# Performance work log

Hardware: AMD Instinct MI355X
Metric: run time of the kernel (lower is better)

Reference implementation:

```python
import jax, jax.numpy as jnp
import numpy as np

N_NODES = 50000
N_EDGES = 500000
D_MODEL = 128
D_INNER = 256
N_EXPERT = 64
TOP_K = 2
CAP_FACTOR = 2  # capacity factor for expert dispatch (fastmoe has no drop; factor 2 is ample for ~uniform gates)
BN_EPS = 1e-5


def setup_inputs() -> dict:
    key = jax.random.key(0)
    ks = jax.random.split(key, 12)
    d, h, E = D_MODEL, D_INNER, N_EXPERT
    return {
        "feats": jax.random.normal(ks[0], (N_NODES, d), jnp.float32),
        "edge_src": jax.random.randint(ks[1], (N_EDGES,), 0, N_NODES),
        "edge_dst": jax.random.randint(ks[2], (N_EDGES,), 0, N_NODES),
        "W_conv": jax.random.normal(ks[3], (d, d), jnp.float32) / np.sqrt(d),
        "b_conv": jnp.zeros((d,), jnp.float32),
        "gate_W": jax.random.normal(ks[4], (d, E), jnp.float32) / np.sqrt(d),
        "gate_b": jnp.zeros((E,), jnp.float32),
        "W1": jax.random.normal(ks[5], (E, d, h), jnp.float32) / np.sqrt(d),
        "b1": jnp.zeros((E, h), jnp.float32),
        "W2": jax.random.normal(ks[6], (E, h, d), jnp.float32) / np.sqrt(h),
        "b2": jnp.zeros((E, d), jnp.float32),
        "bn_gamma": jnp.ones((d,), jnp.float32),
        "bn_beta": jnp.zeros((d,), jnp.float32),
    }


def _gcn_conv(feats, edge_src, edge_dst, W_conv, b_conv):
    # symmetric-normalized sum aggregation over edge list
    n = feats.shape[0]
    ones = jnp.ones_like(edge_dst, dtype=feats.dtype)
    deg = jax.ops.segment_sum(ones, edge_dst, num_segments=n)
    deg = jnp.maximum(deg, 1.0)
    inv_sqrt = jax.lax.rsqrt(deg)
    norm = inv_sqrt[edge_src] * inv_sqrt[edge_dst]          # [Ed]
    msgs = feats[edge_src] * norm[:, None]                  # [Ed, d]
    agg = jax.ops.segment_sum(msgs, edge_dst, num_segments=n)
    return agg @ W_conv + b_conv


def _moe_ffn(x, gate_W, gate_b, W1, b1, W2, b2):
    # fastmoe NaiveGate: top-k of linear gate, softmax over the top-k scores
    T, d = x.shape
    E, h = W1.shape[0], W1.shape[2]
    scores = x @ gate_W + gate_b                            # [T, E]
    topv, topi = jax.lax.top_k(scores, TOP_K)               # [T, k]
    gw = jax.nn.softmax(topv, axis=-1)                      # [T, k]

    P = T * TOP_K
    eid = topi.reshape(P)                                   # expert id per (token, slot)
    x_rep = jnp.repeat(x, TOP_K, axis=0)                    # [P, d]

    onehot = jax.nn.one_hot(eid, E, dtype=jnp.int32)        # [P, E]
    pos = jnp.sum(jnp.cumsum(onehot, axis=0) * onehot, axis=-1) - 1  # rank within expert
    C = CAP_FACTOR * int(np.ceil(P / E))
    valid = pos < C
    slot = eid * C + jnp.where(valid, pos, 0)               # [P]

    buf = jnp.zeros((E * C, d), x.dtype).at[slot].add(
        jnp.where(valid[:, None], x_rep, 0.0))
    buf = buf.reshape(E, C, d)
    hact = jax.nn.gelu(jnp.einsum('ecd,edh->ech', buf, W1) + b1[:, None, :],
                       approximate=False)
    y = jnp.einsum('ech,ehd->ecd', hact, W2) + b2[:, None, :]
    y_pairs = y.reshape(E * C, d)[slot] * valid[:, None].astype(x.dtype)  # [P, d]
    y_pairs = y_pairs.reshape(T, TOP_K, d)
    return jnp.einsum('tk,tkd->td', gw, y_pairs)


def _batchnorm(x, gamma, beta):
    mean = jnp.mean(x, axis=0)
    var = jnp.mean(jnp.square(x - mean), axis=0)  # biased, as torch BN training
    return (x - mean) * jax.lax.rsqrt(var + BN_EPS) * gamma + beta


def reference(feats, edge_src, edge_dst, W_conv, b_conv, gate_W, gate_b,
              W1, b1, W2, b2, bn_gamma, bn_beta):
    new_feats = _gcn_conv(feats, edge_src, edge_dst, W_conv, b_conv)
    core = _moe_ffn(new_feats, gate_W, gate_b, W1, b1, W2, b2)
    # dropout p=0.0 -> identity; BN(inp + core_out)
    return _batchnorm(new_feats + core, bn_gamma, bn_beta)
```

## Files before the change

kernel.cpp:

```cpp
#include <hip/hip_runtime.h>
#include <math.h>

#define N_NODES 50000
#define N_EDGES 500000
#define D 128
#define H 256
#define NE 64
#define TOPK 2
#define NPAIR (N_NODES * TOPK)
#define CAP 3126
#define TILE_R 32
#define BQ 16
#define BN_NBLK 128
#define BN_ROWS ((N_NODES + BN_NBLK - 1) / BN_NBLK)

typedef __attribute__((ext_vector_type(8))) short s16x8;
typedef __attribute__((ext_vector_type(4))) float f32x4;

__device__ __forceinline__ unsigned short f2bf(float f) {
    unsigned u = __float_as_uint(f);
    unsigned r = (u + 0x7fffu + ((u >> 16) & 1u)) >> 16;
    return (unsigned short)r;
}
__device__ __forceinline__ float bf2f(unsigned short u) {
    return __uint_as_float(((unsigned)u) << 16);
}

__device__ __forceinline__ float gelu_f(float x) {
    float u = 0.70710678118654752f * x;
    float au = fabsf(u);
    float t = 1.0f / fmaf(0.3275911f, au, 1.0f);
    float poly = t * fmaf(t, fmaf(t, fmaf(t, fmaf(t, 1.061405429f, -1.453152027f),
                      1.421413741f), -0.284496736f), 0.254829592f);
    float e = __expf(-u * u);
    float erfa = 1.0f - poly * e;
    float erfu = copysignf(erfa, u);
    return 0.5f * x * (1.0f + erfu);
}

#define DOT2(s, c, xx, ww) {                      \
    float p_ = (xx) * (ww);                       \
    float e1_ = fmaf((xx), (ww), -p_);            \
    float t_ = (s) + p_;                          \
    float z_ = t_ - (s);                          \
    float e2_ = ((s) - (t_ - z_)) + (p_ - z_);    \
    (s) = t_;                                     \
    (c) += e1_ + e2_; }

#define TSUM(s, c, pp) {                          \
    float p_ = (pp);                              \
    float t_ = (s) + p_;                          \
    float z_ = t_ - (s);                          \
    float e2_ = ((s) - (t_ - z_)) + (p_ - z_);    \
    (s) = t_;                                     \
    (c) += e2_; }

#define KAH(s, c, pp) {                           \
    float y_ = (pp) - (c);                        \
    float t_ = (s) + y_;                          \
    (c) = (t_ - (s)) - y_;                        \
    (s) = t_; }

__global__ void k_deg(const int* __restrict__ dst, int* __restrict__ deg) {
    int i = blockIdx.x * blockDim.x + threadIdx.x;
    if (i < N_EDGES) atomicAdd(&deg[dst[i]], 1);
}

__global__ void k_invsqrt(const int* __restrict__ deg, float* __restrict__ invs) {
    int i = blockIdx.x * blockDim.x + threadIdx.x;
    if (i < N_NODES) {
        double d = (double)deg[i];
        if (d < 1.0) d = 1.0;
        invs[i] = (float)(1.0 / sqrt(d));
    }
}

__global__ __launch_bounds__(1024) void k_scan(const int* __restrict__ deg,
                                               int* __restrict__ rowptr) {
    __shared__ int sh[1024];
    int t = threadIdx.x;
    const int chunk = (N_NODES + 1023) / 1024;
    int lo = t * chunk;
    int hi = min(lo + chunk, N_NODES);
    int s = 0;
    for (int i = lo; i < hi; i++) s += deg[i];
    sh[t] = s;
    __syncthreads();
    for (int off = 1; off < 1024; off <<= 1) {
        int v = (t >= off) ? sh[t - off] : 0;
        __syncthreads();
        sh[t] += v;
        __syncthreads();
    }
    int run = (t == 0) ? 0 : sh[t - 1];
    for (int i = lo; i < hi; i++) { rowptr[i] = run; run += deg[i]; }
    if (t == 1023) rowptr[N_NODES] = run;
}

__global__ void k_scatter(const int* __restrict__ src, const int* __restrict__ dst,
                          const int* __restrict__ rowptr, int* __restrict__ cursor,
                          int* __restrict__ csr) {
    int e = blockIdx.x * blockDim.x + threadIdx.x;
    if (e >= N_EDGES) return;
    int d = dst[e];
    int pos = atomicAdd(&cursor[d], 1);
    csr[rowptr[d] + pos] = src[e];
}

__global__ __launch_bounds__(256) void k_gather(const float* __restrict__ feats,
                                                const int* __restrict__ rowptr,
                                                const int* __restrict__ csr,
                                                const float* __restrict__ invs,
                                                float* __restrict__ agg) {
    int node = blockIdx.x * 4 + (threadIdx.x >> 6);
    if (node >= N_NODES) return;
    int lane = threadIdx.x & 63;
    int beg = rowptr[node], end = rowptr[node + 1];
    float wd = invs[node];
    float sx = 0.f, cx = 0.f, sy = 0.f, cy = 0.f;
    int i = beg;
    for (; i + 4 <= end; i += 4) {
        int s0 = csr[i], s1 = csr[i + 1], s2 = csr[i + 2], s3 = csr[i + 3];
        float n0 = invs[s0] * wd, n1 = invs[s1] * wd;
        float n2 = invs[s2] * wd, n3 = invs[s3] * wd;
        float2 f0 = ((const float2*)(feats + (size_t)s0 * D))[lane];
        float2 f1 = ((const float2*)(feats + (size_t)s1 * D))[lane];
        float2 f2 = ((const float2*)(feats + (size_t)s2 * D))[lane];
        float2 f3 = ((const float2*)(feats + (size_t)s3 * D))[lane];
        KAH(sx, cx, n0 * f0.x); KAH(sy, cy, n0 * f0.y);
        KAH(sx, cx, n1 * f1.x); KAH(sy, cy, n1 * f1.y);
        KAH(sx, cx, n2 * f2.x); KAH(sy, cy, n2 * f2.y);
        KAH(sx, cx, n3 * f3.x); KAH(sy, cy, n3 * f3.y);
    }
    for (; i < end; i++) {
        int s = csr[i];
        float nrm = invs[s] * wd;
        float2 f = ((const float2*)(feats + (size_t)s * D))[lane];
        KAH(sx, cx, nrm * f.x);
        KAH(sy, cy, nrm * f.y);
    }
    ((float2*)(agg + (size_t)node * D))[lane] = make_float2(sx, sy);
}

__global__ __launch_bounds__(256) void k_conv(const float* __restrict__ agg,
                                              const float* __restrict__ W,
                                              const float* __restrict__ bias,
                                              float* __restrict__ out) {
    __shared__ float Wl[D * D];
    __shared__ float xl[TILE_R * D];
    int r0 = blockIdx.x * TILE_R;
    int rows = min(TILE_R, N_NODES - r0);
    for (int i = threadIdx.x; i < D * D / 4; i += 256)
        ((float4*)Wl)[i] = ((const float4*)W)[i];
    for (int i = threadIdx.x; i < rows * 32; i += 256) {
        int r = i >> 5, q = i & 31;
        ((float4*)(xl + r * D))[q] = ((const float4*)(agg + (size_t)(r0 + r) * D))[q];
    }
    __syncthreads();
    int c = threadIdx.x & 127;
    int half = threadIdx.x >> 7;
    float acc[16];
#pragma unroll
    for (int j = 0; j < 16; j++) acc[j] = 0.f;
    for (int k = 0; k < D; k++) {
        float w = Wl[k * D + c];
#pragma unroll
        for (int j = 0; j < 16; j++) acc[j] += xl[(half + j * 2) * D + k] * w;
    }
    float b = bias[c];
#pragma unroll
    for (int j = 0; j < 16; j++) {
        int r = half + j * 2;
        if (r < rows) out[(size_t)(r0 + r) * D + c] = acc[j] + b;
    }
}

__global__ __launch_bounds__(256, 4) void k_gate(const float* __restrict__ nf,
                                                 const float* __restrict__ gW,
                                                 const float* __restrict__ gb,
                                                 float* __restrict__ gwout,
                                                 int* __restrict__ topi,
                                                 int* __restrict__ rcnt,
                                                 int* __restrict__ redo) {
    __shared__ float Wl[D * NE];
    __shared__ float xsh[16 * D];
    for (int i = threadIdx.x; i < D * NE / 4; i += 256)
        ((float4*)Wl)[i] = ((const float4*)gW)[i];
    int t_base = blockIdx.x * 16;
    for (int i = threadIdx.x; i < 16 * 32; i += 256) {
        int r = i >> 5, q = i & 31;
        ((float4*)(xsh + r * D))[q] =
            ((const float4*)(nf + (size_t)(t_base + r) * D))[q];
    }
    __syncthreads();

    int wave = threadIdx.x >> 6;
    int lane = threadIdx.x & 63;
    int t0 = t_base + wave * 4;
    const float* xw = xsh + wave * 4 * D;

    float a0 = 0.f, a1 = 0.f, a2 = 0.f, a3 = 0.f;
#pragma unroll 4
    for (int k4 = 0; k4 < D; k4 += 4) {
        float x0[4], x1[4], x2[4], x3[4];
        *(float4*)x0 = *(const float4*)(xw + k4);
        *(float4*)x1 = *(const float4*)(xw + D + k4);
        *(float4*)x2 = *(const float4*)(xw + 2 * D + k4);
        *(float4*)x3 = *(const float4*)(xw + 3 * D + k4);
#pragma unroll
        for (int u = 0; u < 4; u++) {
            float w = Wl[(k4 + u) * NE + lane];
            a0 = fmaf(x0[u], w, a0);
            a1 = fmaf(x1[u], w, a1);
            a2 = fmaf(x2[u], w, a2);
            a3 = fmaf(x3[u], w, a3);
        }
    }
    float gbf = gb[lane];
    float af[4] = {a0 + gbf, a1 + gbf, a2 + gbf, a3 + gbf};

    const float TAU = 2e-4f;

#pragma unroll
    for (int j = 0; j < 4; j++) {
        float sf = (j == 0) ? af[0] : (j == 1) ? af[1] : (j == 2) ? af[2] : af[3];
        int t = t0 + j;

        float v1 = sf; int i1 = lane;
#pragma unroll
        for (int off = 32; off; off >>= 1) {
            float ov = __shfl_xor(v1, off);
            int   oi = __shfl_xor(i1, off);
            if (ov > v1 || (ov == v1 && oi < i1)) { v1 = ov; i1 = oi; }
        }
        float v2 = (lane == i1) ? -INFINITY : sf; int i2 = lane;
#pragma unroll
        for (int off = 32; off; off >>= 1) {
            float ov = __shfl_xor(v2, off);
            int   oi = __shfl_xor(i2, off);
            if (ov > v2 || (ov == v2 && oi < i2)) { v2 = ov; i2 = oi; }
        }
        float v3 = (lane == i1 || lane == i2) ? -INFINITY : sf;
#pragma unroll
        for (int off = 32; off; off >>= 1)
            v3 = fmaxf(v3, __shfl_xor(v3, off));

        if (lane == 0) {
            float dd = v2 - v1;
            float e2 = expf(dd);
            float g0 = 1.0f / (1.0f + e2);
            gwout[2 * t] = g0;
            gwout[2 * t + 1] = e2 * g0;
            topi[2 * t] = i1;
            topi[2 * t + 1] = i2;
            if ((v1 - v2 <= TAU) || (v2 - v3 <= TAU)) {
                int slot = atomicAdd(rcnt, 1);
                redo[slot] = t;
            }
        }
    }
}

__global__ __launch_bounds__(256) void k_gfix(const float* __restrict__ nf,
                                              const float* __restrict__ gW,
                                              const float* __restrict__ gb,
                                              const int* __restrict__ rcnt,
                                              const int* __restrict__ redo,
                                              float* __restrict__ gwout,
                                              int* __restrict__ topi) {
    int nredo = *rcnt;
    int lane = threadIdx.x & 63;
    int widx = blockIdx.x * 4 + (threadIdx.x >> 6);
    float gbf = gb[lane];
    for (int i = widx; i < nredo; i += gridDim.x * 4) {
        int t = redo[i];
        const float* xr = nf + (size_t)t * D;
        float s = 0.f, c = 0.f;
        for (int k = 0; k < D; k++)
            DOT2(s, c, xr[k], gW[k * NE + lane]);
        TSUM(s, c, gbf);
        float vv = s + c, rr = (s - vv) + c;

        float a1v = vv, a1r = rr; int i1 = lane;
#pragma unroll
        for (int off = 32; off; off >>= 1) {
            float ov = __shfl_xor(a1v, off);
            float orr = __shfl_xor(a1r, off);
            int   oi = __shfl_xor(i1, off);
            bool gt = (ov > a1v) || (ov == a1v && (orr > a1r || (orr == a1r && oi < i1)));
            if (gt) { a1v = ov; a1r = orr; i1 = oi; }
        }
        bool ex = (lane == i1);
        float a2v = ex ? -INFINITY : vv;
        float a2r = ex ? 0.f : rr;
        int i2 = lane;
#pragma unroll
        for (int off = 32; off; off >>= 1) {
            float ov = __shfl_xor(a2v, off);
            float orr = __shfl_xor(a2r, off);
            int   oi = __shfl_xor(i2, off);
            bool gt = (ov > a2v) || (ov == a2v && (orr > a2r || (orr == a2r && oi < i2)));
            if (gt) { a2v = ov; a2r = orr; i2 = oi; }
        }

        if (lane == 0) {
            float dd = (a2v - a1v) + (a2r - a1r);
            float e2 = expf(dd);
            float g0 = 1.0f / (1.0f + e2);
            gwout[2 * t] = g0;
            gwout[2 * t + 1] = e2 * g0;
            topi[2 * t] = i1;
            topi[2 * t + 1] = i2;
        }
    }
}

__global__ __launch_bounds__(1024) void k_disp(const int* __restrict__ topi,
                                               int* __restrict__ cnt,
                                               int* __restrict__ plist) {
    __shared__ int lcnt[NE];
    __shared__ int lbase[NE];
    int tid = threadIdx.x;
    if (tid < NE) lcnt[tid] = 0;
    __syncthreads();
    int p = blockIdx.x * 1024 + tid;
    int e = 0, lr = 0;
    bool act = (p < NPAIR);
    if (act) {
        e = topi[p];
        lr = atomicAdd(&lcnt[e], 1);
    }
    __syncthreads();
    if (tid < NE) {
        int n = lcnt[tid];
        lbase[tid] = n ? atomicAdd(&cnt[tid], n) : 0;
    }
    __syncthreads();
    if (act) {
        int slot = lbase[e] + lr;
        if (slot < CAP) plist[e * CAP + slot] = p;
    }
}

__global__ __launch_bounds__(256) void k_wconv(const float* __restrict__ W1,
                                               const float* __restrict__ W2,
                                               unsigned short* __restrict__ w1c,
                                               unsigned short* __restrict__ w2c) {
    int gid = blockIdx.x * 256 + threadIdx.x;
    const int NW1 = NE * 4 * 256 * 4;
    if (gid < NW1) {
        int lhi = gid & 3, h = (gid >> 2) & 255, ks = (gid >> 10) & 3, e = gid >> 12;
        int d0 = ks * 32 + lhi * 8;
        unsigned short v[8] __attribute__((aligned(16)));
#pragma unroll
        for (int j = 0; j < 8; j++)
            v[j] = f2bf(W1[((size_t)e * D + d0 + j) * H + h]);
        *(int4*)(w1c + (size_t)gid * 8) = *(int4*)v;
    } else {
        int g = gid - NW1;
        int lhi = g & 3, d = (g >> 2) & 127, ks = (g >> 9) & 7, e = g >> 12;
        int h0 = ks * 32 + lhi * 8;
        unsigned short v[8] __attribute__((aligned(16)));
#pragma unroll
        for (int j = 0; j < 8; j++)
            v[j] = f2bf(W2[((size_t)e * H + h0 + j) * D + d]);
        *(int4*)(w2c + (size_t)g * 8) = *(int4*)v;
    }
}

__global__ __launch_bounds__(512, 4) void k_moe(const float* __restrict__ nf,
                                                const int* __restrict__ cnt,
                                                const int* __restrict__ plist,
                                                const unsigned short* __restrict__ w1c,
                                                const float* __restrict__ b1,
                                                const unsigned short* __restrict__ w2c,
                                                const float* __restrict__ b2,
                                                const float* __restrict__ gwbuf,
                                                unsigned short* __restrict__ ybuf) {
    __shared__ __align__(16) char smem[32768];
    const int XA = 0, HL = 8192, YB = 24576;
    int e = blockIdx.x & 63;
    int q = blockIdx.x >> 6;
    int n = min(cnt[e], CAP);
    int ntile = (n + TILE_R - 1) / TILE_R;
    if (q >= ntile) return;
    int tid = threadIdx.x;

    int wv = tid >> 6, lane = tid & 63;
    int lhi = lane >> 4, llo = lane & 15;
    int sr = tid >> 4, ss = tid & 15;
    f32x4 zero = {0.f, 0.f, 0.f, 0.f};

    s16x8 w1f[4][2];
#pragma unroll
    for (int ks = 0; ks < 4; ks++)
#pragma unroll
        for (int nt = 0; nt < 2; nt++) {
            int h = wv * 32 + nt * 16 + llo;
            w1f[ks][nt] = *(const s16x8*)(w1c +
                ((size_t)e * 4096 + (ks * 256 + h) * 4 + lhi) * 8);
        }
    s16x8 w2f[8];
    {
        int d = wv * 16 + llo;
#pragma unroll
        for (int ks = 0; ks < 8; ks++)
            w2f[ks] = *(const s16x8*)(w2c +
                ((size_t)e * 4096 + (ks * 128 + d) * 4 + lhi) * 8);
    }

    float vals[8];
    auto loadt = [&](int rt2, float* v) {
        bool ok = false;
        if (rt2 < ntile) {
            int rows2 = min(TILE_R, n - rt2 * TILE_R);
            if (sr < rows2) {
                int p = plist[e * CAP + rt2 * TILE_R + sr];
                const float4* xr = (const float4*)(nf + (size_t)(p >> 1) * D + ss * 8);
                *(float4*)(v + 0) = xr[0];
                *(float4*)(v + 4) = xr[1];
                ok = true;
            }
        }
        if (!ok) {
#pragma unroll
            for (int k = 0; k < 8; k++) v[k] = 0.f;
        }
    };
    loadt(q, vals);

    for (int rt = q; rt < ntile; rt += BQ) {
        int r0 = rt * TILE_R;
        int rows = min(TILE_R, n - r0);

        {
            unsigned short hb[8] __attribute__((aligned(16)));
#pragma unroll
            for (int k = 0; k < 8; k++) hb[k] = f2bf(vals[k]);
            *(int4*)(smem + XA + sr * 256 + ((ss * 16) ^ ((sr & 7) << 4))) = *(int4*)hb;
        }
        __syncthreads();

        loadt(rt + BQ, vals);

        f32x4 acc1[2][2];
#pragma unroll
        for (int mt = 0; mt < 2; mt++)
#pragma unroll
            for (int nt = 0; nt < 2; nt++) acc1[mt][nt] = zero;
#pragma unroll
        for (int ks = 0; ks < 4; ks++) {
            int kb = ks * 64 + lhi * 16;
            s16x8 a0 = *(const s16x8*)(smem + XA + llo * 256        + (kb ^ ((llo & 7) << 4)));
            s16x8 a1 = *(const s16x8*)(smem + XA + (llo + 16) * 256 + (kb ^ ((llo & 7) << 4)));
#pragma unroll
            for (int nt = 0; nt < 2; nt++) {
                acc1[0][nt] = __builtin_amdgcn_mfma_f32_16x16x32_bf16(a0, w1f[ks][nt], acc1[0][nt], 0, 0, 0);
                acc1[1][nt] = __builtin_amdgcn_mfma_f32_16x16x32_bf16(a1, w1f[ks][nt], acc1[1][nt], 0, 0, 0);
            }
        }

#pragma unroll
        for (int mt = 0; mt < 2; mt++)
#pragma unroll
            for (int nt = 0; nt < 2; nt++)
#pragma unroll
                for (int r = 0; r < 4; r++) {
                    int m = mt * 16 + lhi * 4 + r;
                    int hc = wv * 32 + nt * 16 + llo;
                    float hv = acc1[mt][nt][r] + b1[e * H + hc];
                    *(unsigned short*)(smem + HL + m * 512 + ((hc * 2) ^ ((m & 7) << 4))) =
                        f2bf(gelu_f(hv));
                }
        __syncthreads();

        f32x4 acc2[2];
        acc2[0] = zero; acc2[1] = zero;
#pragma unroll
        for (int ks = 0; ks < 8; ks++) {
            int kb = ks * 64 + lhi * 16;
            s16x8 a0 = *(const s16x8*)(smem + HL + llo * 512        + (kb ^ ((llo & 7) << 4)));
            s16x8 a1 = *(const s16x8*)(smem + HL + (llo + 16) * 512 + (kb ^ ((llo & 7) << 4)));
            acc2[0] = __builtin_amdgcn_mfma_f32_16x16x32_bf16(a0, w2f[ks], acc2[0], 0, 0, 0);
            acc2[1] = __builtin_amdgcn_mfma_f32_16x16x32_bf16(a1, w2f[ks], acc2[1], 0, 0, 0);
        }

        {
            int d = wv * 16 + llo;
            float bb = b2[e * D + d];
#pragma unroll
            for (int mt = 0; mt < 2; mt++)
#pragma unroll
                for (int r = 0; r < 4; r++) {
                    int m = mt * 16 + lhi * 4 + r;
                    *(unsigned short*)(smem + YB + m * 256 + ((d * 2) ^ ((m & 7) << 4))) =
                        f2bf(acc2[mt][r] + bb);
                }
        }
        __syncthreads();

        if (sr < rows) {
            int p = plist[e * CAP + r0 + sr];
            float gw = gwbuf[p];
            unsigned short yv[8] __attribute__((aligned(16)));
            *(int4*)yv = *(const int4*)(smem + YB + sr * 256 + ((ss * 16) ^ ((sr & 7) << 4)));
#pragma unroll
            for (int k = 0; k < 8; k++) yv[k] = f2bf(gw * bf2f(yv[k]));
            *(int4*)(ybuf + (size_t)p * D + ss * 8) = *(int4*)yv;
        }
    }
}

__global__ __launch_bounds__(256) void k_bnpart(const float* __restrict__ nf,
                                                const unsigned short* __restrict__ ybuf,
                                                double* __restrict__ part) {
    int blk = blockIdx.x;
    int col = threadIdx.x & 127;
    int half = threadIdx.x >> 7;
    int r0 = blk * BN_ROWS;
    int r1 = min(r0 + BN_ROWS, N_NODES);
    double s = 0.0, ss = 0.0;
    for (int r = r0 + half; r < r1; r += 2) {
        float v32 = nf[(size_t)r * D + col]
                  + bf2f(ybuf[(size_t)(2 * r) * D + col])
                  + bf2f(ybuf[(size_t)(2 * r + 1) * D + col]);
        double v = (double)v32;
        s += v; ss += v * v;
    }
    __shared__ double sh[2][256];
    sh[0][threadIdx.x] = s; sh[1][threadIdx.x] = ss;
    __syncthreads();
    if (threadIdx.x < 128) {
        part[(size_t)blk * 256 + col]       = sh[0][col] + sh[0][col + 128];
        part[(size_t)blk * 256 + 128 + col] = sh[1][col] + sh[1][col + 128];
    }
}

__global__ void k_bnstats(const double* __restrict__ part,
                          const float* __restrict__ gamma,
                          float* __restrict__ stats) {
    int col = threadIdx.x;
    double s = 0.0, ss = 0.0;
    for (int b = 0; b < BN_NBLK; b++) {
        s  += part[(size_t)b * 256 + col];
        ss += part[(size_t)b * 256 + 128 + col];
    }
    double mean = s / (double)N_NODES;
    double var = ss / (double)N_NODES - mean * mean;
    stats[col] = (float)mean;
    stats[128 + col] = gamma[col] * (float)(1.0 / sqrt(var + 1e-5));
}

__global__ __launch_bounds__(256) void k_bnapply(const unsigned short* __restrict__ ybuf,
                                                 const float* __restrict__ stats,
                                                 const float* __restrict__ beta,
                                                 float* __restrict__ out) {
    int i = blockIdx.x * blockDim.x + threadIdx.x;
    if (i >= N_NODES * (D / 4)) return;
    int t = i >> 5;
    int q = i & 31;
    int c0 = q * 4;
    float4 v  = ((float4*)out)[i];
    short4 y0v = *(const short4*)(ybuf + (size_t)(2 * t) * D + c0);
    short4 y1v = *(const short4*)(ybuf + (size_t)(2 * t + 1) * D + c0);
    float4 r;
    r.x = (v.x + bf2f((unsigned short)y0v.x) + bf2f((unsigned short)y1v.x) - stats[c0 + 0]) * stats[128 + c0 + 0] + beta[c0 + 0];
    r.y = (v.y + bf2f((unsigned short)y0v.y) + bf2f((unsigned short)y1v.y) - stats[c0 + 1]) * stats[128 + c0 + 1] + beta[c0 + 1];
    r.z = (v.z + bf2f((unsigned short)y0v.z) + bf2f((unsigned short)y1v.z) - stats[c0 + 2]) * stats[128 + c0 + 2] + beta[c0 + 2];
    r.w = (v.w + bf2f((unsigned short)y0v.w) + bf2f((unsigned short)y1v.w) - stats[c0 + 3]) * stats[128 + c0 + 3] + beta[c0 + 3];
    ((float4*)out)[i] = r;
}

extern "C" void kernel_launch(void* const* d_in, const int* in_sizes, int n_in,
                              void* d_out, int out_size, void* d_ws, size_t ws_size,
                              hipStream_t stream) {
    const float* feats   = (const float*)d_in[0];
    const int*   esrc    = (const int*)d_in[1];
    const int*   edst    = (const int*)d_in[2];
    const float* W_conv  = (const float*)d_in[3];
    const float* b_conv  = (const float*)d_in[4];
    const float* gate_W  = (const float*)d_in[5];
    const float* gate_b  = (const float*)d_in[6];
    const float* W1      = (const float*)d_in[7];
    const float* b1      = (const float*)d_in[8];
    const float* W2      = (const float*)d_in[9];
    const float* b2      = (const float*)d_in[10];
    const float* bn_g    = (const float*)d_in[11];
    const float* bn_b    = (const float*)d_in[12];
    float* out = (float*)d_out;

    char* ws = (char*)d_ws;
    size_t off = 0;
    auto rup = [](size_t x) { return (x + 255) & ~(size_t)255; };
    int*    deg    = (int*)   (ws + off); off += rup((size_t)N_NODES * 4);
    int*    cursor = (int*)   (ws + off); off += rup((size_t)N_NODES * 4);
    int*    cnt    = (int*)   (ws + off); off += 256;
    int*    rcnt   = (int*)   (ws + off); off += 256;
    size_t zero_bytes = off;
    float*  invs   = (float*) (ws + off); off += rup((size_t)N_NODES * 4);
    int*    rowptr = (int*)   (ws + off); off += rup((size_t)(N_NODES + 1) * 4);
    int*    csr    = (int*)   (ws + off); off += rup((size_t)N_EDGES * 4);
    float*  gwbuf  = (float*) (ws + off); off += rup((size_t)NPAIR * 4);
    int*    topi   = (int*)   (ws + off); off += rup((size_t)NPAIR * 4);
    int*    redo   = (int*)   (ws + off); off += rup((size_t)N_NODES * 4);
    int*    plist  = (int*)   (ws + off); off += rup((size_t)NE * CAP * 4);
    double* part   = (double*)(ws + off); off += rup((size_t)BN_NBLK * 256 * 8);
    float*  stats  = (float*) (ws + off); off += 1024;
    unsigned short* w1c = (unsigned short*)(ws + off); off += rup((size_t)NE * D * H * 2);
    unsigned short* w2c = (unsigned short*)(ws + off); off += rup((size_t)NE * D * H * 2);
    unsigned short* ybuf = (unsigned short*)(ws + off); off += rup((size_t)NPAIR * D * 2);
    float*  agg    = (float*)ybuf;
    (void)ws_size; (void)in_sizes; (void)n_in; (void)out_size;

    hipMemsetAsync(d_ws, 0, zero_bytes, stream);

    k_wconv<<<2 * NE * 4 * 256 * 4 / 256, 256, 0, stream>>>(W1, W2, w1c, w2c);
    k_deg<<<(N_EDGES + 255) / 256, 256, 0, stream>>>(edst, deg);
    k_invsqrt<<<(N_NODES + 255) / 256, 256, 0, stream>>>(deg, invs);
    k_scan<<<1, 1024, 0, stream>>>(deg, rowptr);
    k_scatter<<<(N_EDGES + 255) / 256, 256, 0, stream>>>(esrc, edst, rowptr, cursor, csr);
    k_gather<<<(N_NODES + 3) / 4, 256, 0, stream>>>(feats, rowptr, csr, invs, agg);
    k_conv<<<(N_NODES + TILE_R - 1) / TILE_R, 256, 0, stream>>>(agg, W_conv, b_conv, out);
    k_gate<<<N_NODES / 16, 256, 0, stream>>>(out, gate_W, gate_b, gwbuf, topi, rcnt, redo);
    k_gfix<<<128, 256, 0, stream>>>(out, gate_W, gate_b, rcnt, redo, gwbuf, topi);
    k_disp<<<(NPAIR + 1023) / 1024, 1024, 0, stream>>>(topi, cnt, plist);
    k_moe<<<NE * BQ, 512, 0, stream>>>(out, cnt, plist, w1c, b1, w2c, b2, gwbuf, ybuf);
    k_bnpart<<<BN_NBLK, 256, 0, stream>>>(out, ybuf, part);
    k_bnstats<<<1, 128, 0, stream>>>(part, bn_g, stats);
    k_bnapply<<<(N_NODES * (D / 4) + 255) / 256, 256, 0, stream>>>(ybuf, stats, bn_b, out);
}
```

Before: 461.2 us.

## Move GCN linear layer to split-bf16 MFMA and fold residual sum into BN partial pass

The scalar FP32 conv GEMM, which staged a full 64KB copy of W in LDS per block, is replaced by an MFMA kernel. Both activations and weights are split into hi and lo bf16 parts, and three MFMAs per tile approximate FP32 accuracy. A small pre-kernel packs W_conv into fragment-ordered hi/lo arrays. Separately, the BN partial pass now writes the summed nf+y back to out, so the apply pass no longer re-reads the bf16 expert outputs. This trades an extra write in bnpart for fewer reads in bnapply.

```diff
diff --git a/kernel.cpp b/kernel.cpp
--- a/kernel.cpp
+++ b/kernel.cpp
@@ -142,36 +142,110 @@
     ((float2*)(agg + (size_t)node * D))[lane] = make_float2(sx, sy);
 }
 
-__global__ __launch_bounds__(256) void k_conv(const float* __restrict__ agg,
-                                              const float* __restrict__ W,
-                                              const float* __restrict__ bias,
-                                              float* __restrict__ out) {
-    __shared__ float Wl[D * D];
-    __shared__ float xl[TILE_R * D];
+__global__ __launch_bounds__(256) void k_wcsplit(const float* __restrict__ W,
+                                                 unsigned short* __restrict__ whi,
+                                                 unsigned short* __restrict__ wlo) {
+    int u = blockIdx.x * 256 + threadIdx.x;
+    int lhi = u & 3, c = (u >> 2) & 127, ks = u >> 9;
+    int k0 = ks * 32 + lhi * 8;
+    unsigned short vh[8] __attribute__((aligned(16)));
+    unsigned short vl[8] __attribute__((aligned(16)));
+#pragma unroll
+    for (int j = 0; j < 8; j++) {
+        float x = W[(size_t)(k0 + j) * D + c];
+        unsigned short h = f2bf(x);
+        vh[j] = h;
+        vl[j] = f2bf(x - bf2f(h));
+    }
+    *(int4*)(whi + (size_t)u * 8) = *(int4*)vh;
+    *(int4*)(wlo + (size_t)u * 8) = *(int4*)vl;
+}
+
+__global__ __launch_bounds__(512, 4) void k_conv(const float* __restrict__ agg,
+                                                 const unsigned short* __restrict__ whi,
+                                                 const unsigned short* __restrict__ wlo,
+                                                 const float* __restrict__ bias,
+                                                 float* __restrict__ out) {
+    __shared__ __align__(16) char smem[32768];
+    const int XH = 0, XL = 8192, YB = 16384;
     int r0 = blockIdx.x * TILE_R;
     int rows = min(TILE_R, N_NODES - r0);
-    for (int i = threadIdx.x; i < D * D / 4; i += 256)
-        ((float4*)Wl)[i] = ((const float4*)W)[i];
-    for (int i = threadIdx.x; i < rows * 32; i += 256) {
-        int r = i >> 5, q = i & 31;
-        ((float4*)(xl + r * D))[q] = ((const float4*)(agg + (size_t)(r0 + r) * D))[q];
+    int tid = threadIdx.x;
+    int wv = tid >> 6, lane = tid & 63;
+    int lhi = lane >> 4, llo = lane & 15;
+    int sr = tid >> 4, ss = tid & 15;
+    f32x4 zero = {0.f, 0.f, 0.f, 0.f};
+
+    int c = wv * 16 + llo;
+    s16x8 whf[4], wlf[4];
+#pragma unroll
+    for (int ks = 0; ks < 4; ks++) {
+        size_t u = ((size_t)(ks * 128 + c) * 4 + lhi) * 8;
+        whf[ks] = *(const s16x8*)(whi + u);
+        wlf[ks] = *(const s16x8*)(wlo + u);
+    }
+
+    {
+        float v[8];
+        if (sr < rows) {
+            const float4* xr = (const float4*)(agg + (size_t)(r0 + sr) * D + ss * 8);
+            *(float4*)(v + 0) = xr[0];
+            *(float4*)(v + 4) = xr[1];
+        } else {
+#pragma unroll
+            for (int k = 0; k < 8; k++) v[k] = 0.f;
+        }
+        unsigned short hb[8] __attribute__((aligned(16)));
+        unsigned short lb[8] __attribute__((aligned(16)));
+#pragma unroll
+        for (int k = 0; k < 8; k++) {
+            unsigned short h = f2bf(v[k]);
+            hb[k] = h;
+            lb[k] = f2bf(v[k] - bf2f(h));
+        }
+        int swz = (sr & 7) << 4;
+        *(int4*)(smem + XH + sr * 256 + ((ss * 16) ^ swz)) = *(int4*)hb;
+        *(int4*)(smem + XL + sr * 256 + ((ss * 16) ^ swz)) = *(int4*)lb;
     }
     __syncthreads();
-    int c = threadIdx.x & 127;
-    int half = threadIdx.x >> 7;
-    float acc[16];
-#pragma unroll
-    for (int j = 0; j < 16; j++) acc[j] = 0.f;
-    for (int k = 0; k < D; k++) {
-        float w = Wl[k * D + c];
-#pragma unroll
-        for (int j = 0; j < 16; j++) acc[j] += xl[(half + j * 2) * D + k] * w;
-    }
-    float b = bias[c];
-#pragma unroll
-    for (int j = 0; j < 16; j++) {
-        int r = half + j * 2;
-        if (r < rows) out[(size_t)(r0 + r) * D + c] = acc[j] + b;
+
+    f32x4 acc[2];
+    acc[0] = zero; acc[1] = zero;
+#pragma unroll
+    for (int ks = 0; ks < 4; ks++) {
+        int kb = ks * 64 + lhi * 16;
+        int sw0 = (llo & 7) << 4;
+        s16x8 ah0 = *(const s16x8*)(smem + XH + llo * 256        + (kb ^ sw0));
+        s16x8 ah1 = *(const s16x8*)(smem + XH + (llo + 16) * 256 + (kb ^ sw0));
+        s16x8 al0 = *(const s16x8*)(smem + XL + llo * 256        + (kb ^ sw0));
+        s16x8 al1 = *(const s16x8*)(smem + XL + (llo + 16) * 256 + (kb ^ sw0));
+        acc[0] = __builtin_amdgcn_mfma_f32_16x16x32_bf16(ah0, whf[ks], acc[0], 0, 0, 0);
+        acc[0] = __builtin_amdgcn_mfma_f32_16x16x32_bf16(ah0, wlf[ks], acc[0], 0, 0, 0);
+        acc[0] = __builtin_amdgcn_mfma_f32_16x16x32_bf16(al0, whf[ks], acc[0], 0, 0, 0);
+        acc[1] = __builtin_amdgcn_mfma_f32_16x16x32_bf16(ah1, whf[ks], acc[1], 0, 0, 0);
+        acc[1] = __builtin_amdgcn_mfma_f32_16x16x32_bf16(ah1, wlf[ks], acc[1], 0, 0, 0);
+        acc[1] = __builtin_amdgcn_mfma_f32_16x16x32_bf16(al1, whf[ks], acc[1], 0, 0, 0);
+    }
+
+    {
+        float bb = bias[c];
+#pragma unroll
+        for (int mt = 0; mt < 2; mt++)
+#pragma unroll
+            for (int r = 0; r < 4; r++) {
+                int m = mt * 16 + lhi * 4 + r;
+                *(float*)(smem + YB + m * 512 + ((c * 4) ^ ((m & 7) << 4))) = acc[mt][r] + bb;
+            }
+    }
+    __syncthreads();
+
+    if (sr < rows) {
+        int swz = (sr & 7) << 4;
+        int4 a = *(const int4*)(smem + YB + sr * 512 + ((ss * 32) ^ swz));
+        int4 b = *(const int4*)(smem + YB + sr * 512 + ((ss * 32 + 16) ^ swz));
+        float4* op = (float4*)(out + (size_t)(r0 + sr) * D + ss * 8);
+        op[0] = *(float4*)&a;
+        op[1] = *(float4*)&b;
     }
 }
 
@@ -511,7 +585,7 @@
     }
 }
 
-__global__ __launch_bounds__(256) void k_bnpart(const float* __restrict__ nf,
+__global__ __launch_bounds__(256) void k_bnpart(float* __restrict__ nf,
                                                 const unsigned short* __restrict__ ybuf,
                                                 double* __restrict__ part) {
     int blk = blockIdx.x;
@@ -524,6 +598,7 @@
         float v32 = nf[(size_t)r * D + col]
                   + bf2f(ybuf[(size_t)(2 * r) * D + col])
                   + bf2f(ybuf[(size_t)(2 * r + 1) * D + col]);
+        nf[(size_t)r * D + col] = v32;
         double v = (double)v32;
         s += v; ss += v * v;
     }
@@ -551,23 +626,19 @@
     stats[128 + col] = gamma[col] * (float)(1.0 / sqrt(var + 1e-5));
 }
 
-__global__ __launch_bounds__(256) void k_bnapply(const unsigned short* __restrict__ ybuf,
-                                                 const float* __restrict__ stats,
+__global__ __launch_bounds__(256) void k_bnapply(const float* __restrict__ stats,
                                                  const float* __restrict__ beta,
                                                  float* __restrict__ out) {
     int i = blockIdx.x * blockDim.x + threadIdx.x;
     if (i >= N_NODES * (D / 4)) return;
-    int t = i >> 5;
     int q = i & 31;
     int c0 = q * 4;
-    float4 v  = ((float4*)out)[i];
-    short4 y0v = *(const short4*)(ybuf + (size_t)(2 * t) * D + c0);
-    short4 y1v = *(const short4*)(ybuf + (size_t)(2 * t + 1) * D + c0);
+    float4 z = ((const float4*)out)[i];
     float4 r;
-    r.x = (v.x + bf2f((unsigned short)y0v.x) + bf2f((unsigned short)y1v.x) - stats[c0 + 0]) * stats[128 + c0 + 0] + beta[c0 + 0];
-    r.y = (v.y + bf2f((unsigned short)y0v.y) + bf2f((unsigned short)y1v.y) - stats[c0 + 1]) * stats[128 + c0 + 1] + beta[c0 + 1];
-    r.z = (v.z + bf2f((unsigned short)y0v.z) + bf2f((unsigned short)y1v.z) - stats[c0 + 2]) * stats[128 + c0 + 2] + beta[c0 + 2];
-    r.w = (v.w + bf2f((unsigned short)y0v.w) + bf2f((unsigned short)y1v.w) - stats[c0 + 3]) * stats[128 + c0 + 3] + beta[c0 + 3];
+    r.x = (z.x - stats[c0 + 0]) * stats[128 + c0 + 0] + beta[c0 + 0];
+    r.y = (z.y - stats[c0 + 1]) * stats[128 + c0 + 1] + beta[c0 + 1];
+    r.z = (z.z - stats[c0 + 2]) * stats[128 + c0 + 2] + beta[c0 + 2];
+    r.w = (z.w - stats[c0 + 3]) * stats[128 + c0 + 3] + beta[c0 + 3];
     ((float4*)out)[i] = r;
 }
 
@@ -606,8 +677,10 @@
     int*    plist  = (int*)   (ws + off); off += rup((size_t)NE * CAP * 4);
     double* part   = (double*)(ws + off); off += rup((size_t)BN_NBLK * 256 * 8);
     float*  stats  = (float*) (ws + off); off += 1024;
-    unsigned short* w1c = (unsigned short*)(ws + off); off += rup((size_t)NE * D * H * 2);
-    unsigned short* w2c = (unsigned short*)(ws + off); off += rup((size_t)NE * D * H * 2);
+    unsigned short* w1c  = (unsigned short*)(ws + off); off += rup((size_t)NE * D * H * 2);
+    unsigned short* w2c  = (unsigned short*)(ws + off); off += rup((size_t)NE * D * H * 2);
+    unsigned short* wchi = (unsigned short*)(ws + off); off += rup((size_t)D * D * 2);
+    unsigned short* wclo = (unsigned short*)(ws + off); off += rup((size_t)D * D * 2);
     unsigned short* ybuf = (unsigned short*)(ws + off); off += rup((size_t)NPAIR * D * 2);
     float*  agg    = (float*)ybuf;
     (void)ws_size; (void)in_sizes; (void)n_in; (void)out_size;
@@ -615,17 +688,18 @@
     hipMemsetAsync(d_ws, 0, zero_bytes, stream);
 
     k_wconv<<<2 * NE * 4 * 256 * 4 / 256, 256, 0, stream>>>(W1, W2, w1c, w2c);
+    k_wcsplit<<<8, 256, 0, stream>>>(W_conv, wchi, wclo);
     k_deg<<<(N_EDGES + 255) / 256, 256, 0, stream>>>(edst, deg);
     k_invsqrt<<<(N_NODES + 255) / 256, 256, 0, stream>>>(deg, invs);
     k_scan<<<1, 1024, 0, stream>>>(deg, rowptr);
     k_scatter<<<(N_EDGES + 255) / 256, 256, 0, stream>>>(esrc, edst, rowptr, cursor, csr);
     k_gather<<<(N_NODES + 3) / 4, 256, 0, stream>>>(feats, rowptr, csr, invs, agg);
-    k_conv<<<(N_NODES + TILE_R - 1) / TILE_R, 256, 0, stream>>>(agg, W_conv, b_conv, out);
+    k_conv<<<(N_NODES + TILE_R - 1) / TILE_R, 512, 0, stream>>>(agg, wchi, wclo, b_conv, out);
     k_gate<<<N_NODES / 16, 256, 0, stream>>>(out, gate_W, gate_b, gwbuf, topi, rcnt, redo);
     k_gfix<<<128, 256, 0, stream>>>(out, gate_W, gate_b, rcnt, redo, gwbuf, topi);
     k_disp<<<(NPAIR + 1023) / 1024, 1024, 0, stream>>>(topi, cnt, plist);
     k_moe<<<NE * BQ, 512, 0, stream>>>(out, cnt, plist, w1c, b1, w2c, b2, gwbuf, ybuf);
     k_bnpart<<<BN_NBLK, 256, 0, stream>>>(out, ybuf, part);
     k_bnstats<<<1, 128, 0, stream>>>(part, bn_g, stats);
-    k_bnapply<<<(N_NODES * (D / 4) + 255) / 256, 256, 0, stream>>>(ybuf, stats, bn_b, out);
-}
+    k_bnapply<<<(N_NODES * (D / 4) + 255) / 256, 256, 0, stream>>>(stats, bn_b, out);
+}
```

After: 417.7 us. 9.4% less time.
